# Kernel optimization log

Measured on AMD Instinct MI355X. Metric: run time of the kernel, lower is better.

The kernel has to match this reference:

```python
import jax, jax.numpy as jnp
import numpy as np
from jax import lax

N = 200000
CIN = 64
COUT = 128
K = 27  # 3^3 kernel offsets
EPS = 1e-5


def _make_rulebook(key, n, k):
    ki, km = jax.random.split(key)
    idx = jax.random.randint(ki, (k, n), 0, n, dtype=jnp.int32)
    keep = jax.random.uniform(km, (k, n)) < 0.5
    idx = jnp.where(keep, idx, -1)
    # center offset is always the voxel itself (submanifold conv)
    idx = idx.at[k // 2].set(jnp.arange(n, dtype=jnp.int32))
    return idx


def setup_inputs() -> dict:
    key = jax.random.key(0)
    ks = jax.random.split(key, 8)
    feats = jax.random.normal(ks[0], (N, CIN), dtype=jnp.float32)
    nbr1 = _make_rulebook(ks[1], N, K)
    nbr2 = _make_rulebook(ks[2], N, K)
    W1 = jax.random.normal(ks[3], (K, CIN, COUT), dtype=jnp.float32) * 0.05
    W2 = jax.random.normal(ks[4], (K, COUT, COUT), dtype=jnp.float32) * 0.05
    Wd = jax.random.normal(ks[5], (CIN, COUT), dtype=jnp.float32) * 0.05
    g1 = jnp.ones((COUT,), jnp.float32); b1 = jnp.zeros((COUT,), jnp.float32)
    g2 = jnp.ones((COUT,), jnp.float32); b2 = jnp.zeros((COUT,), jnp.float32)
    gd = jnp.ones((COUT,), jnp.float32); bd = jnp.zeros((COUT,), jnp.float32)
    return dict(feats=feats, nbr1=nbr1, nbr2=nbr2, W1=W1, W2=W2, Wd=Wd,
                g1=g1, b1=b1, g2=g2, b2=b2, gd=gd, bd=bd)


def sparse_conv(feats, W, nbr):
    """Rulebook sparse conv: gather neighbors per offset, GEMM, accumulate.
    feats: [N, Cin]; W: [K, Cin, Cout]; nbr: [K, N] int (-1 = missing)."""
    n = feats.shape[0]
    acc0 = jnp.zeros((n, W.shape[-1]), feats.dtype)

    def body(acc, xs):
        idx, Wk = xs  # [N], [Cin, Cout]
        valid = (idx >= 0).astype(feats.dtype)[:, None]
        g = feats[jnp.clip(idx, 0)] * valid  # masked gather [N, Cin]
        return acc + g @ Wk, None

    out, _ = lax.scan(body, acc0, (nbr, W))
    return out


def batchnorm(x, gamma, beta):
    mean = jnp.mean(x, axis=0)
    var = jnp.var(x, axis=0)
    return (x - mean) * lax.rsqrt(var + EPS) * gamma + beta


def reference(feats, nbr1, nbr2, W1, W2, Wd, g1, b1, g2, b2, gd, bd):
    h = sparse_conv(feats, W1, nbr1)
    h = jax.nn.relu(batchnorm(h, g1, b1))
    h = sparse_conv(h, W2, nbr2)
    h = batchnorm(h, g2, b2)
    skip = batchnorm(feats @ Wd, gd, bd)  # 1x1 conv downsample (Cin != Cout)
    return jax.nn.relu(h + skip)
```

## Files before the change

kernel.cpp:

```cpp
#include <hip/hip_runtime.h>
#include <stdint.h>

#define KOFF 27
#define CIN 64
#define COUT 128
#define EPS 1e-5f

using frag_ab = __attribute__((ext_vector_type(8))) short;
using frag_cd = __attribute__((ext_vector_type(4))) float;

__device__ __forceinline__ float bf2f(unsigned short u) {
  union { unsigned int i; float f; } x; x.i = ((unsigned int)u) << 16; return x.f;
}
__device__ __forceinline__ unsigned short f2bf(float f) {
  union { float f; unsigned int i; } x; x.f = f;
  unsigned int u = x.i;
  u += 0x7fffu + ((u >> 16) & 1u);
  return (unsigned short)(u >> 16);
}

__device__ __forceinline__ void gld16(const void* gptr, void* lptr) {
  __builtin_amdgcn_global_load_lds(
      (const __attribute__((address_space(1))) unsigned int*)gptr,
      (__attribute__((address_space(3))) unsigned int*)lptr, 16, 0, 0);
}

template <int CI, bool GATHER, bool OF32>
__global__ __launch_bounds__(256, 3) void conv_kernel(
    const unsigned short* __restrict__ X, const int* __restrict__ nbr,
    const unsigned short* __restrict__ Wt, void* __restrict__ Yv,
    const unsigned short* __restrict__ zpage, float* __restrict__ sums,
    int n, int koff) {
  constexpr int SUB = CI / 64;
  __shared__ unsigned short Alds[2][128 * 64];

  const int tid = threadIdx.x;
  const int lane = tid & 63;
  const int wave = tid >> 6;
  const int row0 = blockIdx.x * 128;
  const int wrow = (wave >> 1) * 64;
  const int wcol = (wave & 1) * 64;
  const int m = lane & 15;
  const int q = lane >> 4;

  frag_cd acc[4][4];
#pragma unroll
  for (int i = 0; i < 4; ++i)
#pragma unroll
    for (int j = 0; j < 4; ++j) acc[i][j] = (frag_cd){0.f, 0.f, 0.f, 0.f};

  frag_ab b[2][4];
  int idxc[4];

  auto load_idx = [&](int ko, int (&dst)[4]) {
#pragma unroll
    for (int c = 0; c < 4; ++c) {
      const int grow = row0 + wave * 32 + c * 8 + (lane >> 3);
      int v = -1;
      if (grow < n) v = GATHER ? nbr[(size_t)ko * n + grow] : grow;
      dst[c] = v;
    }
  };
  auto stageA = [&](int buf, const int (&idx)[4], int sub) {
    const int cho = sub * 64 + ((lane & 7) ^ (lane >> 3)) * 8;
#pragma unroll
    for (int c = 0; c < 4; ++c) {
      const unsigned short* ga =
          (idx[c] >= 0) ? X + (size_t)idx[c] * CI + cho : zpage;
      gld16(ga, &Alds[buf][(wave * 32 + c * 8) * 64]);
    }
  };
  auto loadB = [&](int t) {
#pragma unroll
    for (int kk = 0; kk < 2; ++kk) {
      const unsigned short* base =
          Wt + (size_t)(2 * t + kk) * 4096 + q * 1024 + m * 8;
#pragma unroll
      for (int j = 0; j < 4; ++j)
        b[kk][j] = *(const frag_ab*)(base + (wcol + 16 * j) * 8);
    }
  };
  auto do_mfma = [&](int abuf) {
#pragma unroll
    for (int kk = 0; kk < 2; ++kk) {
      frag_ab a[4];
#pragma unroll
      for (int i = 0; i < 4; ++i) {
        const int row = wrow + 16 * i + m;
        a[i] = *(const frag_ab*)(
            &Alds[abuf][row * 64 + ((kk * 4 + q) ^ (m & 7)) * 8]);
      }
#pragma unroll
      for (int i = 0; i < 4; ++i)
#pragma unroll
        for (int j = 0; j < 4; ++j)
          acc[i][j] = __builtin_amdgcn_mfma_f32_16x16x32_bf16(
              a[i], b[kk][j], acc[i][j], 0, 0, 0);
    }
  };

  const int T = koff * SUB;
  {
    int idx0[4];
    load_idx(0, idx0);
    stageA(0, idx0, 0);
    if (SUB == 2) {
#pragma unroll
      for (int c = 0; c < 4; ++c) idxc[c] = idx0[c];
    } else {
      load_idx(1, idxc);
    }
  }

  for (int t = 0; t < T; ++t) {
    __syncthreads();
    const int u = t + 1;
    if (u < T) {
      stageA(u & 1, idxc, (SUB == 2) ? (u & 1) : 0);
      const int w2 = t + 2;
      if (w2 < T && (SUB == 1 || (w2 & 1) == 0))
        load_idx((SUB == 2) ? (w2 >> 1) : w2, idxc);
    }
    loadB(t);
    do_mfma(t & 1);
  }

#pragma unroll
  for (int j = 0; j < 4; ++j) {
    float s = 0.f, qq = 0.f;
#pragma unroll
    for (int i = 0; i < 4; ++i)
#pragma unroll
      for (int r = 0; r < 4; ++r) {
        float v = acc[i][j][r];
        s += v; qq += v * v;
      }
    s += __shfl_xor(s, 16); s += __shfl_xor(s, 32);
    qq += __shfl_xor(qq, 16); qq += __shfl_xor(qq, 32);
    if (lane < 16) {
      const int col = wcol + 16 * j + lane;
      atomicAdd(&sums[col], s);
      atomicAdd(&sums[COUT + col], qq);
    }
  }

#pragma unroll
  for (int i = 0; i < 4; ++i) {
#pragma unroll
    for (int r = 0; r < 4; ++r) {
      const int grow = row0 + wrow + 16 * i + q * 4 + r;
      if (grow < n) {
#pragma unroll
        for (int j = 0; j < 4; ++j) {
          const int gcol = wcol + 16 * j + m;
          if (OF32)
            ((float*)Yv)[(size_t)grow * COUT + gcol] = acc[i][j][r];
          else
            ((unsigned short*)Yv)[(size_t)grow * COUT + gcol] = f2bf(acc[i][j][r]);
        }
      }
    }
  }
}

__global__ __launch_bounds__(256, 2) void convskip_kernel(
    const float* __restrict__ feats, const float* __restrict__ Wd,
    unsigned short* __restrict__ featsb, unsigned short* __restrict__ sX,
    float* __restrict__ sums, int n) {
  __shared__ unsigned short Alds[2][128 * 32];
  const int tid = threadIdx.x;
  const int lane = tid & 63;
  const int wave = tid >> 6;
  const int row0 = blockIdx.x * 128;
  const int wrow = (wave >> 1) * 64;
  const int wcol = (wave & 1) * 64;
  const int m = lane & 15;
  const int q = lane >> 4;

#pragma unroll
  for (int c = 0; c < 4; ++c) {
    int u = c * 256 + tid;
    int kc = u >> 9;
    int v = u & 511;
    int row = v >> 2;
    int s = v & 3;
    int g = s ^ ((row >> 1) & 3);
    int grow = row0 + row;
    uint4 out = make_uint4(0u, 0u, 0u, 0u);
    if (grow < n) {
      const float* p = feats + (size_t)grow * 64 + kc * 32 + g * 8;
      float4 lo = *(const float4*)p;
      float4 hi = *(const float4*)(p + 4);
      out.x = (unsigned)f2bf(lo.x) | ((unsigned)f2bf(lo.y) << 16);
      out.y = (unsigned)f2bf(lo.z) | ((unsigned)f2bf(lo.w) << 16);
      out.z = (unsigned)f2bf(hi.x) | ((unsigned)f2bf(hi.y) << 16);
      out.w = (unsigned)f2bf(hi.z) | ((unsigned)f2bf(hi.w) << 16);
      *(uint4*)(featsb + (size_t)grow * 64 + kc * 32 + g * 8) = out;
    }
    *(uint4*)(&Alds[kc][row * 32 + s * 8]) = out;
  }
  __syncthreads();

  frag_cd acc[4][4];
#pragma unroll
  for (int i = 0; i < 4; ++i)
#pragma unroll
    for (int j = 0; j < 4; ++j) acc[i][j] = (frag_cd){0.f, 0.f, 0.f, 0.f};

#pragma unroll
  for (int kc = 0; kc < 2; ++kc) {
    frag_ab b[4];
#pragma unroll
    for (int j = 0; j < 4; ++j) {
      const int co = wcol + 16 * j + m;
#pragma unroll
      for (int e = 0; e < 8; ++e)
        b[j][e] = (short)f2bf(Wd[(size_t)(kc * 32 + q * 8 + e) * 128 + co]);
    }
    frag_ab a[4];
#pragma unroll
    for (int i = 0; i < 4; ++i) {
      const int row = wrow + 16 * i + m;
      a[i] = *(const frag_ab*)(&Alds[kc][row * 32 + (q ^ ((row >> 1) & 3)) * 8]);
    }
#pragma unroll
    for (int i = 0; i < 4; ++i)
#pragma unroll
      for (int j = 0; j < 4; ++j)
        acc[i][j] = __builtin_amdgcn_mfma_f32_16x16x32_bf16(a[i], b[j],
                                                            acc[i][j], 0, 0, 0);
  }

#pragma unroll
  for (int j = 0; j < 4; ++j) {
    float s = 0.f, qq = 0.f;
#pragma unroll
    for (int i = 0; i < 4; ++i)
#pragma unroll
      for (int r = 0; r < 4; ++r) {
        float v = acc[i][j][r];
        s += v; qq += v * v;
      }
    s += __shfl_xor(s, 16); s += __shfl_xor(s, 32);
    qq += __shfl_xor(qq, 16); qq += __shfl_xor(qq, 32);
    if (lane < 16) {
      const int col = wcol + 16 * j + lane;
      atomicAdd(&sums[col], s);
      atomicAdd(&sums[COUT + col], qq);
    }
  }

#pragma unroll
  for (int i = 0; i < 4; ++i) {
#pragma unroll
    for (int r = 0; r < 4; ++r) {
      const int grow = row0 + wrow + 16 * i + q * 4 + r;
      if (grow < n) {
#pragma unroll
        for (int j = 0; j < 4; ++j)
          sX[(size_t)grow * COUT + wcol + 16 * j + m] = f2bf(acc[i][j][r]);
      }
    }
  }
}

__global__ void prep_kernel(const float* __restrict__ W1,
                            const float* __restrict__ W2,
                            unsigned short* __restrict__ Wt1,
                            unsigned short* __restrict__ Wt2,
                            float* __restrict__ zbase,
                            float* __restrict__ zpage) {
  const int NZ = 768 + 64;
  const int NW1 = KOFF * CIN * 128;
  const int NW2 = KOFF * COUT * 128;
  int gid = blockIdx.x * 256 + threadIdx.x;
  if (gid < NZ) {
    if (gid < 768) zbase[gid] = 0.f; else zpage[gid - 768] = 0.f;
    return;
  }
  gid -= NZ;
  const float* src;
  unsigned short* dst;
  int ci;
  if (gid < NW1) { src = W1; dst = Wt1; ci = CIN; }
  else if (gid < NW1 + NW2) { gid -= NW1; src = W2; dst = Wt2; ci = COUT; }
  else return;
  int e = gid & 7;
  int co = (gid >> 3) & 127;
  int qq = (gid >> 10) & 3;
  int slab = gid >> 12;
  int nc = ci >> 5;
  int ko = slab / nc;
  int kc = slab - ko * nc;
  int cin = kc * 32 + qq * 8 + e;
  dst[gid] = f2bf(src[((size_t)ko * ci + cin) * 128 + co]);
}

__global__ void norm_relu_kernel(unsigned short* __restrict__ x,
                                 const float* __restrict__ sums,
                                 const float* __restrict__ gamma,
                                 const float* __restrict__ beta,
                                 int n, int total8) {
  __shared__ float sc[COUT], sh[COUT];
  const int tid = threadIdx.x;
  if (tid < COUT) {
    float inv_n = 1.f / (float)n;
    float mean = sums[tid] * inv_n;
    float var = sums[COUT + tid] * inv_n - mean * mean;
    float s = gamma[tid] * rsqrtf(var + EPS);
    sc[tid] = s;
    sh[tid] = beta[tid] - mean * s;
  }
  __syncthreads();
  int gid = blockIdx.x * 256 + tid;
  if (gid >= total8) return;
  size_t i = (size_t)gid * 8;
  int c0 = (int)(i & 127);
  uint4 v = *(const uint4*)(x + i);
  unsigned int w[4] = {v.x, v.y, v.z, v.w};
  unsigned int wo[4];
#pragma unroll
  for (int e = 0; e < 4; ++e) {
    int c = c0 + 2 * e;
    float f0 = bf2f((unsigned short)(w[e] & 0xffffu));
    float f1 = bf2f((unsigned short)(w[e] >> 16));
    f0 = fmaxf(f0 * sc[c] + sh[c], 0.f);
    f1 = fmaxf(f1 * sc[c + 1] + sh[c + 1], 0.f);
    wo[e] = (unsigned int)f2bf(f0) | ((unsigned int)f2bf(f1) << 16);
  }
  *(uint4*)(x + i) = make_uint4(wo[0], wo[1], wo[2], wo[3]);
}

__global__ void final_kernel(float* __restrict__ h2,
                             const unsigned short* __restrict__ s,
                             const float* __restrict__ sums2,
                             const float* __restrict__ sumsd,
                             const float* __restrict__ g2,
                             const float* __restrict__ b2,
                             const float* __restrict__ gd,
                             const float* __restrict__ bd,
                             int n, int total4) {
  __shared__ float sc2[COUT], sh2[COUT], scd[COUT], shd[COUT];
  const int tid = threadIdx.x;
  if (tid < COUT) {
    float inv_n = 1.f / (float)n;
    float mean = sums2[tid] * inv_n;
    float var = sums2[COUT + tid] * inv_n - mean * mean;
    float sa = g2[tid] * rsqrtf(var + EPS);
    sc2[tid] = sa;
    sh2[tid] = b2[tid] - mean * sa;
    mean = sumsd[tid] * inv_n;
    var = sumsd[COUT + tid] * inv_n - mean * mean;
    float sb = gd[tid] * rsqrtf(var + EPS);
    scd[tid] = sb;
    shd[tid] = bd[tid] - mean * sb;
  }
  __syncthreads();
  int gid = blockIdx.x * 256 + tid;
  if (gid >= total4) return;
  size_t i = (size_t)gid * 4;
  int c = (int)(i & 127);
  float4 a = *(const float4*)(h2 + i);
  uint2 sv = *(const uint2*)(s + i);
  float b0 = bf2f((unsigned short)(sv.x & 0xffffu));
  float b1 = bf2f((unsigned short)(sv.x >> 16));
  float b2f = bf2f((unsigned short)(sv.y & 0xffffu));
  float b3 = bf2f((unsigned short)(sv.y >> 16));
  float4 o;
  o.x = fmaxf(a.x * sc2[c] + sh2[c] + b0 * scd[c] + shd[c], 0.f);
  o.y = fmaxf(a.y * sc2[c + 1] + sh2[c + 1] + b1 * scd[c + 1] + shd[c + 1], 0.f);
  o.z = fmaxf(a.z * sc2[c + 2] + sh2[c + 2] + b2f * scd[c + 2] + shd[c + 2], 0.f);
  o.w = fmaxf(a.w * sc2[c + 3] + sh2[c + 3] + b3 * scd[c + 3] + shd[c + 3], 0.f);
  *(float4*)(h2 + i) = o;
}

extern "C" void kernel_launch(void* const* d_in, const int* in_sizes, int n_in,
                              void* d_out, int out_size, void* d_ws,
                              size_t ws_size, hipStream_t stream) {
  (void)n_in; (void)out_size; (void)ws_size;
  const float* feats = (const float*)d_in[0];
  const int* nbr1 = (const int*)d_in[1];
  const int* nbr2 = (const int*)d_in[2];
  const float* W1 = (const float*)d_in[3];
  const float* W2 = (const float*)d_in[4];
  const float* Wd = (const float*)d_in[5];
  const float* g1 = (const float*)d_in[6];
  const float* b1 = (const float*)d_in[7];
  const float* g2 = (const float*)d_in[8];
  const float* b2 = (const float*)d_in[9];
  const float* gd = (const float*)d_in[10];
  const float* bd = (const float*)d_in[11];

  const int n = in_sizes[0] / CIN;

  char* ws = (char*)d_ws;
  unsigned short* Wt1 = (unsigned short*)(ws);
  unsigned short* Wt2 = (unsigned short*)(ws + 442368);
  unsigned short* h1 = (unsigned short*)(ws + 1343488);
  unsigned short* sX = (unsigned short*)(ws + 52543488);
  float* sums1 = (float*)(ws + 103743488);
  float* sums2 = sums1 + 2 * COUT;
  float* sumsd = sums1 + 4 * COUT;
  unsigned short* zpage = (unsigned short*)(ws + 103743488 + 8192);

  float* h2 = (float*)d_out;
  unsigned short* featsb = (unsigned short*)((char*)d_out + 76800000);

  const int prep_units = (768 + 64) + KOFF * CIN * 128 + KOFF * COUT * 128;
  prep_kernel<<<(prep_units + 255) / 256, 256, 0, stream>>>(
      W1, W2, Wt1, Wt2, sums1, (float*)zpage);

  const int mblocks = (n + 127) / 128;
  convskip_kernel<<<mblocks, 256, 0, stream>>>(feats, Wd, featsb, sX, sumsd, n);

  conv_kernel<CIN, true, false><<<mblocks, 256, 0, stream>>>(
      featsb, nbr1, Wt1, h1, zpage, sums1, n, KOFF);

  const int total8 = n * COUT / 8;
  norm_relu_kernel<<<(total8 + 255) / 256, 256, 0, stream>>>(h1, sums1, g1, b1, n, total8);

  conv_kernel<COUT, true, true><<<mblocks, 256, 0, stream>>>(
      h1, nbr2, Wt2, h2, zpage, sums2, n, KOFF);

  const int total4 = n * COUT / 4;
  final_kernel<<<(total4 + 255) / 256, 256, 0, stream>>>(
      h2, sX, sums2, sumsd, g2, b2, gd, bd, n, total4);
}
```

Measured before the change: 664.7 us.

## Replace direct global-to-LDS gather with register-staged two-deep prefetch

Swaps the global_load_lds async copies for ordinary 16-byte global loads into registers, issued two steps ahead, and writes them to LDS one step ahead of use. The aim is a deeper gather pipeline so that random-row load latency overlaps with more MFMA work. In exchange the kernel holds 8 extra uint4 registers per thread, which may hurt occupancy under the launch bounds of 3 blocks, and it adds LDS store instructions.

Result: slower. 1.304 ms (+96.2%).

```diff
diff --git a/kernel.cpp b/kernel.cpp
--- a/kernel.cpp
+++ b/kernel.cpp
@@ -17,12 +17,6 @@
   unsigned int u = x.i;
   u += 0x7fffu + ((u >> 16) & 1u);
   return (unsigned short)(u >> 16);
-}
-
-__device__ __forceinline__ void gld16(const void* gptr, void* lptr) {
-  __builtin_amdgcn_global_load_lds(
-      (const __attribute__((address_space(1))) unsigned int*)gptr,
-      (__attribute__((address_space(3))) unsigned int*)lptr, 16, 0, 0);
 }
 
 template <int CI, bool GATHER, bool OF32>
@@ -42,6 +36,7 @@
   const int wcol = (wave & 1) * 64;
   const int m = lane & 15;
   const int q = lane >> 4;
+  const int g8 = ((lane & 7) ^ (lane >> 3)) * 8;
 
   frag_cd acc[4][4];
 #pragma unroll
@@ -50,6 +45,7 @@
     for (int j = 0; j < 4; ++j) acc[i][j] = (frag_cd){0.f, 0.f, 0.f, 0.f};
 
   frag_ab b[2][4];
+  uint4 P0[4], P1[4];
   int idxc[4];
 
   auto load_idx = [&](int ko, int (&dst)[4]) {
@@ -61,14 +57,19 @@
       dst[c] = v;
     }
   };
-  auto stageA = [&](int buf, const int (&idx)[4], int sub) {
-    const int cho = sub * 64 + ((lane & 7) ^ (lane >> 3)) * 8;
+  auto issueA = [&](uint4 (&P)[4], int u, const int (&idx)[4]) {
+    const int ch = (SUB == 2 ? (u & 1) * 64 : 0) + g8;
 #pragma unroll
     for (int c = 0; c < 4; ++c) {
       const unsigned short* ga =
-          (idx[c] >= 0) ? X + (size_t)idx[c] * CI + cho : zpage;
-      gld16(ga, &Alds[buf][(wave * 32 + c * 8) * 64]);
-    }
+          (idx[c] >= 0) ? X + (size_t)idx[c] * CI + ch : zpage;
+      P[c] = *(const uint4*)ga;
+    }
+  };
+  auto writeA = [&](int buf, const uint4 (&P)[4]) {
+#pragma unroll
+    for (int c = 0; c < 4; ++c)
+      *(uint4*)(&Alds[buf][(wave * 32 + c * 8) * 64 + lane * 8]) = P[c];
   };
   auto loadB = [&](int t) {
 #pragma unroll
@@ -100,26 +101,34 @@
   };
 
   const int T = koff * SUB;
+
+  load_idx(0, idxc);
+  issueA(P0, 0, idxc);
+  if (SUB == 1) {
+    if (1 < koff) load_idx(1, idxc);
+    issueA(P1, 1, idxc);
+  } else {
+    issueA(P1, 1, idxc);
+  }
   {
-    int idx0[4];
-    load_idx(0, idx0);
-    stageA(0, idx0, 0);
-    if (SUB == 2) {
-#pragma unroll
-      for (int c = 0; c < 4; ++c) idxc[c] = idx0[c];
-    } else {
-      load_idx(1, idxc);
-    }
-  }
+    const int ko2 = (SUB == 2) ? 1 : 2;
+    if (ko2 < koff) load_idx(ko2, idxc);
+  }
+  writeA(0, P0);
 
   for (int t = 0; t < T; ++t) {
     __syncthreads();
-    const int u = t + 1;
-    if (u < T) {
-      stageA(u & 1, idxc, (SUB == 2) ? (u & 1) : 0);
-      const int w2 = t + 2;
-      if (w2 < T && (SUB == 1 || (w2 & 1) == 0))
-        load_idx((SUB == 2) ? (w2 >> 1) : w2, idxc);
+    const int u1 = t + 1;
+    if (u1 < T) {
+      if (u1 & 1) writeA(1, P1); else writeA(0, P0);
+    }
+    const int u2 = t + 2;
+    if (u2 < T) {
+      if (u2 & 1) issueA(P1, u2, idxc); else issueA(P0, u2, idxc);
+      if (SUB == 1 || (u2 & 1)) {
+        const int kon = (SUB == 2) ? ((u2 + 1) >> 1) : (u2 + 1);
+        if (kon < koff) load_idx(kon, idxc);
+      }
     }
     loadB(t);
     do_mfma(t & 1);
```
